# Kernel tuning notes

Measured on AMD Instinct MI355X. Metric: run time of the kernel, lower is better.

Reference implementation:

```python
import jax, jax.numpy as jnp
import numpy as np

B, T, C, H = 4096, 4, 1024, 8
DH = C // H
SCALE = DH ** -0.5
LN_EPS = 1e-5


def setup_inputs() -> dict:
    key = jax.random.key(0)
    k1, k2, k3 = jax.random.split(key, 3)
    feats = jax.random.normal(k1, (B, T, C), dtype=jnp.float32)
    Wqkv = jax.random.normal(k2, (T, C, 3 * C), dtype=jnp.float32) * 0.02
    bqkv = jnp.zeros((T, 3 * C), dtype=jnp.float32)
    Wproj = jax.random.normal(k3, (T, C, C), dtype=jnp.float32) * 0.02
    bproj = jnp.zeros((T, C), dtype=jnp.float32)
    gamma = jnp.ones((C,), dtype=jnp.float32)
    beta = jnp.zeros((C,), dtype=jnp.float32)
    return {"feats": feats, "Wqkv": Wqkv, "bqkv": bqkv,
            "Wproj": Wproj, "bproj": bproj, "gamma": gamma, "beta": beta}


def reference(feats, Wqkv, bqkv, Wproj, bproj, gamma, beta):
    # Grouped per-task QKV projection: [B,T,C] x [T,C,3C] -> [B,T,3C]
    qkv = jnp.einsum('btc,tcd->btd', feats, Wqkv) + bqkv
    q, k, v = jnp.split(qkv, 3, axis=-1)           # each [B,T,C]
    q = q.reshape(B, T, H, DH)
    k = k.reshape(B, T, H, DH)
    v = v.reshape(B, T, H, DH)
    # Cross-task attention: scores[b, query_task, key_task, head]
    scores = jnp.einsum('bqhd,bkhd->bqkh', q, k) * SCALE
    attn = jax.nn.softmax(scores, axis=2)          # softmax over key-task dim
    ctx = jnp.einsum('bqkh,bkhd->bqhd', attn, v)   # [B,T,H,DH]
    ctx = ctx.reshape(B, T, C)
    # Grouped per-task output projection (dropout is identity in eval)
    ctx = jnp.einsum('btc,tcd->btd', ctx, Wproj) + bproj
    # Residual + shared LayerNorm over channel dim
    x = ctx + feats
    mu = jnp.mean(x, axis=-1, keepdims=True)
    var = jnp.mean(jnp.square(x - mu), axis=-1, keepdims=True)
    return (x - mu) * jax.lax.rsqrt(var + LN_EPS) * gamma + beta
```

## Files before the change

### kernel.cpp

```cpp
#include <hip/hip_runtime.h>
#include <hip/hip_bf16.h>
#include <cstdint>
#include <cstddef>

#define B_SZ 4096
#define T_SZ 4
#define C_SZ 1024
#define H_SZ 8
#define DH_SZ 128
#define NQKV 3072
#define SCALE_F 0.08838834764831845f

typedef float f32x4 __attribute__((ext_vector_type(4)));
typedef short s16x8 __attribute__((ext_vector_type(8)));

static __device__ __forceinline__ float bf2f(unsigned short u) {
    union { unsigned int i; float f; } x; x.i = ((unsigned int)u) << 16; return x.f;
}
static __device__ __forceinline__ unsigned short f2bf(float f) {
    union { unsigned int i; float f; } x; x.f = f;
    unsigned int r = x.i + 0x7FFFu + ((x.i >> 16) & 1u);
    return (unsigned short)(r >> 16);
}

typedef const __attribute__((address_space(1))) void* gas_ptr;
typedef __attribute__((address_space(3))) void* las_ptr;
static __device__ __forceinline__ void async16(const void* g, void* l) {
    __builtin_amdgcn_global_load_lds((gas_ptr)g, (las_ptr)l, 16, 0, 0);
}

__global__ __launch_bounds__(256) void cvt_f32_bf16(const float* __restrict__ src,
                                                    unsigned short* __restrict__ dst, int n4) {
    int i = blockIdx.x * 256 + threadIdx.x;
    if (i >= n4) return;
    float4 v = reinterpret_cast<const float4*>(src)[i];
    ushort4 o;
    o.x = f2bf(v.x); o.y = f2bf(v.y); o.z = f2bf(v.z); o.w = f2bf(v.w);
    reinterpret_cast<ushort4*>(dst)[i] = o;
}

__global__ __launch_bounds__(256) void transpose_cvt(const float* __restrict__ src,
                                                     unsigned short* __restrict__ dst,
                                                     int K, int N) {
    __shared__ float tile[32][33];
    const float* s = src + (size_t)blockIdx.z * K * N;
    unsigned short* d = dst + (size_t)blockIdx.z * K * N;
    int n0 = blockIdx.x * 32, k0 = blockIdx.y * 32;
    int tx = threadIdx.x, ty = threadIdx.y;
#pragma unroll
    for (int i = 0; i < 4; i++) {
        int k = k0 + ty + i * 8;
        tile[ty + i * 8][tx] = s[(size_t)k * N + n0 + tx];
    }
    __syncthreads();
#pragma unroll
    for (int i = 0; i < 4; i++) {
        int n = n0 + ty + i * 8;
        d[(size_t)n * K + k0 + tx] = f2bf(tile[tx][ty + i * 8]);
    }
}

template<int NSIZE, int EPI>
__global__ __launch_bounds__(512, 1) void gemm256(
    const unsigned short* __restrict__ A,
    const unsigned short* __restrict__ Bt,
    const float* __restrict__ bias,
    const float* __restrict__ resid,
    unsigned short* __restrict__ out_bf,
    float* __restrict__ out_f)
{
    constexpr int BK  = 64;
    constexpr int NBX = NSIZE / 256;
    constexpr int NBY = B_SZ / 256;
    constexpr int NWG = NBX * NBY * T_SZ;

    __shared__ __align__(16) unsigned short lds[65536];

    const int bid = blockIdx.x;
    const int swz = (bid & 7) * (NWG >> 3) + (bid >> 3);
    const int by  = swz & (NBY - 1);
    const int tmp = swz >> 4;
    const int bx  = tmp % NBX;
    const int t   = tmp / NBX;
    const int m0  = by * 256;
    const int n0  = bx * 256;

    const int tid  = threadIdx.x;
    const int lane = tid & 63;
    const int w    = tid >> 6;
    const int wm   = w >> 2;
    const int wn   = w & 3;
    const int quad = lane >> 4;
    const int l16  = lane & 15;

    const int q0  = w * 128 + lane;
    const int q1  = q0 + 64;
    const int r0  = q0 >> 3, ch0 = (q0 & 7) ^ (r0 & 7);
    const int r1  = q1 >> 3, ch1 = (q1 & 7) ^ (r1 & 7);
    const unsigned short* Abase = A + (size_t)t * C_SZ;
    const unsigned short* Bbase = Bt + (size_t)t * NSIZE * C_SZ;
    const unsigned short* gA0 = Abase + (size_t)(m0 + r0) * (T_SZ * C_SZ) + ch0 * 8;
    const unsigned short* gA1 = Abase + (size_t)(m0 + r1) * (T_SZ * C_SZ) + ch1 * 8;
    const unsigned short* gB0 = Bbase + (size_t)(n0 + r0) * C_SZ + ch0 * 8;
    const unsigned short* gB1 = Bbase + (size_t)(n0 + r1) * C_SZ + ch1 * 8;
    unsigned short* dA0 = &lds[(w * 2 + 0) * 512];
    unsigned short* dA1 = &lds[(w * 2 + 1) * 512];
    unsigned short* dB0 = &lds[32768 + (w * 2 + 0) * 512];
    unsigned short* dB1 = &lds[32768 + (w * 2 + 1) * 512];

#define STG_A(buf, h, kt) do { \
    async16(gA0 + (size_t)(h) * 128 * (T_SZ * C_SZ) + (kt) * BK, dA0 + (buf) * 16384 + (h) * 8192); \
    async16(gA1 + (size_t)(h) * 128 * (T_SZ * C_SZ) + (kt) * BK, dA1 + (buf) * 16384 + (h) * 8192); \
} while (0)
#define STG_B(buf, h, kt) do { \
    async16(gB0 + (size_t)(h) * 128 * C_SZ + (kt) * BK, dB0 + (buf) * 16384 + (h) * 8192); \
    async16(gB1 + (size_t)(h) * 128 * C_SZ + (kt) * BK, dB1 + (buf) * 16384 + (h) * 8192); \
} while (0)

    const int s7   = l16 & 7;
    const int swk0 = ((0 * 4 + quad) ^ s7) * 8;
    const int swk1 = ((1 * 4 + quad) ^ s7) * 8;
    const unsigned short* aR = &lds[wm * 8192 + l16 * 64];
    const unsigned short* bR = &lds[32768 + (wn >> 1) * 8192 + ((wn & 1) * 64 + l16) * 64];

#define LD_A(buf, mh) do { \
    _Pragma("unroll") \
    for (int mi = 0; mi < 4; ++mi) { \
        af[mi][0] = *(const s16x8*)(aR + (buf) * 16384 + ((mh) * 4 + mi) * 1024 + swk0); \
        af[mi][1] = *(const s16x8*)(aR + (buf) * 16384 + ((mh) * 4 + mi) * 1024 + swk1); \
    } \
} while (0)
#define LD_B(buf, nh, dst) do { \
    _Pragma("unroll") \
    for (int ni = 0; ni < 2; ++ni) { \
        dst[ni][0] = *(const s16x8*)(bR + (buf) * 16384 + ((nh) * 2 + ni) * 1024 + swk0); \
        dst[ni][1] = *(const s16x8*)(bR + (buf) * 16384 + ((nh) * 2 + ni) * 1024 + swk1); \
    } \
} while (0)
#define MM(mh, nh, bsrc) do { \
    _Pragma("unroll") \
    for (int mi = 0; mi < 4; ++mi) \
    _Pragma("unroll") \
    for (int ni = 0; ni < 2; ++ni) { \
        acc[(mh) * 4 + mi][(nh) * 2 + ni] = __builtin_amdgcn_mfma_f32_16x16x32_bf16( \
            af[mi][0], bsrc[ni][0], acc[(mh) * 4 + mi][(nh) * 2 + ni], 0, 0, 0); \
        acc[(mh) * 4 + mi][(nh) * 2 + ni] = __builtin_amdgcn_mfma_f32_16x16x32_bf16( \
            af[mi][1], bsrc[ni][1], acc[(mh) * 4 + mi][(nh) * 2 + ni], 0, 0, 0); \
    } \
} while (0)
#define WALL() do { \
    __builtin_amdgcn_s_barrier(); \
    __builtin_amdgcn_sched_barrier(0); \
} while (0)
#define KTILE(buf, kt, SP0, SP23, VMC) do { \
     \
    asm volatile("s_waitcnt vmcnt(" #VMC ")"); \
    __builtin_amdgcn_sched_barrier(0); \
    WALL(); \
    LD_B(buf, 0, bq0); \
    LD_A(buf, 0); \
    LD_B(buf, 1, bq1); \
    if (SP0) STG_A((buf) ^ 1, 1, (kt) + 1); \
    __builtin_amdgcn_s_setprio(1); MM(0, 0, bq0); MM(0, 1, bq1); __builtin_amdgcn_s_setprio(0); \
     \
    WALL(); \
    LD_A(buf, 1); \
    if (SP23) { STG_B(buf, 0, (kt) + 2); STG_A(buf, 0, (kt) + 2); STG_B(buf, 1, (kt) + 2); } \
    __builtin_amdgcn_s_setprio(1); MM(1, 1, bq1); MM(1, 0, bq0); __builtin_amdgcn_s_setprio(0); \
} while (0)

    f32x4 acc[8][4] = {};
    s16x8 af[4][2], bq0[2][2], bq1[2][2];

    STG_A(0, 0, 0); STG_B(0, 0, 0); STG_B(0, 1, 0);
    STG_A(0, 1, 0);
    STG_B(1, 0, 1); STG_A(1, 0, 1); STG_B(1, 1, 1);

#pragma clang loop unroll(disable)
    for (int it = 0; it < 7; ++it) {
        int kt = it * 2;
        KTILE(0, kt,     1, 1, 6);
        KTILE(1, kt + 1, 1, 1, 6);
    }
    KTILE(0, 14, 1, 0, 6);
    KTILE(1, 15, 0, 0, 0);

#undef KTILE
#undef WALL
#undef MM
#undef LD_B
#undef LD_A
#undef STG_B
#undef STG_A

#pragma unroll
    for (int ni = 0; ni < 4; ++ni) {
        int gn = n0 + wn * 64 + ni * 16 + l16;
        float bi = bias[t * NSIZE + gn];
#pragma unroll
        for (int mi = 0; mi < 8; ++mi) {
#pragma unroll
            for (int r = 0; r < 4; ++r) {
                int gm = m0 + wm * 128 + mi * 16 + quad * 4 + r;
                size_t o = (size_t)(gm * T_SZ + t) * NSIZE + gn;
                float v = acc[mi][ni][r] + bi;
                if (EPI == 0) {
                    out_bf[o] = f2bf(v);
                } else {
                    out_f[o] = v + resid[o];
                }
            }
        }
    }
}

__global__ __launch_bounds__(256) void attn_kernel(const unsigned short* __restrict__ qkv,
                                                   unsigned short* __restrict__ ctx) {
    const int tid = threadIdx.x;
    const int li  = tid & 15;
    const int g   = blockIdx.x * 16 + (tid >> 4);
    const int b   = g >> 3, h = g & 7;
    const int d0  = li * 8;

    const unsigned short* base = qkv + (size_t)b * (T_SZ * NQKV) + h * DH_SZ + d0;
    float qf[4][8], kf[4][8], vf[4][8];
#pragma unroll
    for (int i = 0; i < 4; i++) {
        const unsigned short* p = base + (size_t)i * NQKV;
        s16x8 qv = *reinterpret_cast<const s16x8*>(p);
        s16x8 kv = *reinterpret_cast<const s16x8*>(p + C_SZ);
        s16x8 vv = *reinterpret_cast<const s16x8*>(p + 2 * C_SZ);
#pragma unroll
        for (int e = 0; e < 8; e++) {
            qf[i][e] = bf2f((unsigned short)qv[e]);
            kf[i][e] = bf2f((unsigned short)kv[e]);
            vf[i][e] = bf2f((unsigned short)vv[e]);
        }
    }
    float s[4][4];
#pragma unroll
    for (int i = 0; i < 4; i++)
#pragma unroll
        for (int j = 0; j < 4; j++) {
            float p = 0.0f;
#pragma unroll
            for (int e = 0; e < 8; e++) p += qf[i][e] * kf[j][e];
            p += __shfl_xor(p, 8);
            p += __shfl_xor(p, 4);
            p += __shfl_xor(p, 2);
            p += __shfl_xor(p, 1);
            s[i][j] = p * SCALE_F;
        }
#pragma unroll
    for (int i = 0; i < 4; i++) {
        float m = fmaxf(fmaxf(s[i][0], s[i][1]), fmaxf(s[i][2], s[i][3]));
        float e0 = __expf(s[i][0] - m), e1 = __expf(s[i][1] - m);
        float e2 = __expf(s[i][2] - m), e3 = __expf(s[i][3] - m);
        float inv = 1.0f / (e0 + e1 + e2 + e3);
        s[i][0] = e0 * inv; s[i][1] = e1 * inv; s[i][2] = e2 * inv; s[i][3] = e3 * inv;
    }
#pragma unroll
    for (int i = 0; i < 4; i++) {
        s16x8 ov;
#pragma unroll
        for (int e = 0; e < 8; e++) {
            float o = s[i][0] * vf[0][e] + s[i][1] * vf[1][e]
                    + s[i][2] * vf[2][e] + s[i][3] * vf[3][e];
            ov[e] = (short)f2bf(o);
        }
        *reinterpret_cast<s16x8*>(ctx + (size_t)(b * T_SZ + i) * C_SZ + h * DH_SZ + d0) = ov;
    }
}

__global__ __launch_bounds__(256) void ln_kernel(const float* __restrict__ y,
                                                 const float* __restrict__ gamma,
                                                 const float* __restrict__ beta,
                                                 float* __restrict__ out) {
    int row = blockIdx.x;
    int lane = threadIdx.x & 63, wave = threadIdx.x >> 6;
    float4 v = reinterpret_cast<const float4*>(y + (size_t)row * C_SZ)[threadIdx.x];
    float s  = v.x + v.y + v.z + v.w;
    float ss = v.x * v.x + v.y * v.y + v.z * v.z + v.w * v.w;
#pragma unroll
    for (int off = 32; off > 0; off >>= 1) { s += __shfl_xor(s, off); ss += __shfl_xor(ss, off); }
    __shared__ float red[8];
    if (lane == 0) { red[wave] = s; red[wave + 4] = ss; }
    __syncthreads();
    float S  = red[0] + red[1] + red[2] + red[3];
    float SS = red[4] + red[5] + red[6] + red[7];
    float mean = S * (1.0f / C_SZ);
    float var  = SS * (1.0f / C_SZ) - mean * mean;
    float inv  = rsqrtf(var + 1e-5f);
    float4 g  = reinterpret_cast<const float4*>(gamma)[threadIdx.x];
    float4 be = reinterpret_cast<const float4*>(beta)[threadIdx.x];
    float4 o;
    o.x = (v.x - mean) * inv * g.x + be.x;
    o.y = (v.y - mean) * inv * g.y + be.y;
    o.z = (v.z - mean) * inv * g.z + be.z;
    o.w = (v.w - mean) * inv * g.w + be.w;
    reinterpret_cast<float4*>(out + (size_t)row * C_SZ)[threadIdx.x] = o;
}

extern "C" void kernel_launch(void* const* d_in, const int* in_sizes, int n_in,
                              void* d_out, int out_size, void* d_ws, size_t ws_size,
                              hipStream_t stream) {
    const float* feats = (const float*)d_in[0];
    const float* Wqkv  = (const float*)d_in[1];
    const float* bqkv  = (const float*)d_in[2];
    const float* Wproj = (const float*)d_in[3];
    const float* bproj = (const float*)d_in[4];
    const float* gamma = (const float*)d_in[5];
    const float* beta  = (const float*)d_in[6];
    float* out = (float*)d_out;

    char* ws = (char*)d_ws;
    unsigned short* feats_bf = (unsigned short*)(ws);
    unsigned short* wqkv_t   = (unsigned short*)(ws + 33554432);
    unsigned short* wproj_t  = (unsigned short*)(ws + 58720256);
    unsigned short* qkv      = (unsigned short*)(ws + 67108864);
    unsigned short* ctx      = (unsigned short*)(ws + 167772160);
    float* ybuf              = (float*)(ws + 67108864);

    cvt_f32_bf16<<<16384, 256, 0, stream>>>(feats, feats_bf, (B_SZ * T_SZ * C_SZ) / 4);
    transpose_cvt<<<dim3(96, 32, 4), dim3(32, 8), 0, stream>>>(Wqkv, wqkv_t, C_SZ, NQKV);
    transpose_cvt<<<dim3(32, 32, 4), dim3(32, 8), 0, stream>>>(Wproj, wproj_t, C_SZ, C_SZ);

    gemm256<NQKV, 0><<<dim3(768), 512, 0, stream>>>(
        feats_bf, wqkv_t, bqkv, nullptr, qkv, nullptr);

    attn_kernel<<<(B_SZ * H_SZ) / 16, 256, 0, stream>>>(qkv, ctx);

    gemm256<C_SZ, 1><<<dim3(256), 512, 0, stream>>>(
        ctx, wproj_t, bproj, feats, nullptr, ybuf);

    ln_kernel<<<B_SZ * T_SZ, 256, 0, stream>>>(ybuf, gamma, beta, out);
}
```

Before: 405.4 us.

## Emit bf16 from output projection and fuse residual into wave-per-row LayerNorm

The output-projection GEMM now writes bf16 instead of fp32 with a residual read, and the residual add moves into a new LayerNorm kernel that handles one row per wave with no shared-memory reduction. The weight transpose processes 64-row tiles and writes packed ushort2 pairs, and the feature conversion uses a grid-stride loop with fewer blocks. These changes cut GEMM epilogue traffic and launch and synchronisation overhead. Rounding the pre-LayerNorm projection output to bf16 adds some precision loss.

```diff
diff --git a/kernel.cpp b/kernel.cpp
--- a/kernel.cpp
+++ b/kernel.cpp
@@ -31,24 +31,25 @@
 
 __global__ __launch_bounds__(256) void cvt_f32_bf16(const float* __restrict__ src,
                                                     unsigned short* __restrict__ dst, int n4) {
-    int i = blockIdx.x * 256 + threadIdx.x;
-    if (i >= n4) return;
-    float4 v = reinterpret_cast<const float4*>(src)[i];
-    ushort4 o;
-    o.x = f2bf(v.x); o.y = f2bf(v.y); o.z = f2bf(v.z); o.w = f2bf(v.w);
-    reinterpret_cast<ushort4*>(dst)[i] = o;
+    int stride = gridDim.x * 256;
+    for (int i = blockIdx.x * 256 + threadIdx.x; i < n4; i += stride) {
+        float4 v = reinterpret_cast<const float4*>(src)[i];
+        ushort4 o;
+        o.x = f2bf(v.x); o.y = f2bf(v.y); o.z = f2bf(v.z); o.w = f2bf(v.w);
+        reinterpret_cast<ushort4*>(dst)[i] = o;
+    }
 }
 
 __global__ __launch_bounds__(256) void transpose_cvt(const float* __restrict__ src,
                                                      unsigned short* __restrict__ dst,
                                                      int K, int N) {
-    __shared__ float tile[32][33];
+    __shared__ float tile[64][33];
     const float* s = src + (size_t)blockIdx.z * K * N;
     unsigned short* d = dst + (size_t)blockIdx.z * K * N;
-    int n0 = blockIdx.x * 32, k0 = blockIdx.y * 32;
+    int n0 = blockIdx.x * 32, k0 = blockIdx.y * 64;
     int tx = threadIdx.x, ty = threadIdx.y;
 #pragma unroll
-    for (int i = 0; i < 4; i++) {
+    for (int i = 0; i < 8; i++) {
         int k = k0 + ty + i * 8;
         tile[ty + i * 8][tx] = s[(size_t)k * N + n0 + tx];
     }
@@ -56,18 +57,19 @@
 #pragma unroll
     for (int i = 0; i < 4; i++) {
         int n = n0 + ty + i * 8;
-        d[(size_t)n * K + k0 + tx] = f2bf(tile[tx][ty + i * 8]);
-    }
-}
-
-template<int NSIZE, int EPI>
+        ushort2 o;
+        o.x = f2bf(tile[2 * tx][ty + i * 8]);
+        o.y = f2bf(tile[2 * tx + 1][ty + i * 8]);
+        *reinterpret_cast<ushort2*>(&d[(size_t)n * K + k0 + 2 * tx]) = o;
+    }
+}
+
+template<int NSIZE>
 __global__ __launch_bounds__(512, 1) void gemm256(
     const unsigned short* __restrict__ A,
     const unsigned short* __restrict__ Bt,
     const float* __restrict__ bias,
-    const float* __restrict__ resid,
-    unsigned short* __restrict__ out_bf,
-    float* __restrict__ out_f)
+    unsigned short* __restrict__ out_bf)
 {
     constexpr int BK  = 64;
     constexpr int NBX = NSIZE / 256;
@@ -203,12 +205,7 @@
             for (int r = 0; r < 4; ++r) {
                 int gm = m0 + wm * 128 + mi * 16 + quad * 4 + r;
                 size_t o = (size_t)(gm * T_SZ + t) * NSIZE + gn;
-                float v = acc[mi][ni][r] + bi;
-                if (EPI == 0) {
-                    out_bf[o] = f2bf(v);
-                } else {
-                    out_f[o] = v + resid[o];
-                }
+                out_bf[o] = f2bf(acc[mi][ni][r] + bi);
             }
         }
     }
@@ -272,33 +269,47 @@
     }
 }
 
-__global__ __launch_bounds__(256) void ln_kernel(const float* __restrict__ y,
-                                                 const float* __restrict__ gamma,
-                                                 const float* __restrict__ beta,
-                                                 float* __restrict__ out) {
-    int row = blockIdx.x;
-    int lane = threadIdx.x & 63, wave = threadIdx.x >> 6;
-    float4 v = reinterpret_cast<const float4*>(y + (size_t)row * C_SZ)[threadIdx.x];
-    float s  = v.x + v.y + v.z + v.w;
-    float ss = v.x * v.x + v.y * v.y + v.z * v.z + v.w * v.w;
+__global__ __launch_bounds__(256) void ln_fused(const unsigned short* __restrict__ yb,
+                                                const float* __restrict__ feats,
+                                                const float* __restrict__ gamma,
+                                                const float* __restrict__ beta,
+                                                float* __restrict__ out) {
+    const int wave = threadIdx.x >> 6, lane = threadIdx.x & 63;
+    const int row = blockIdx.x * 4 + wave;
+    const unsigned short* yp = yb + (size_t)row * C_SZ;
+    const float* fp = feats + (size_t)row * C_SZ;
+
+    float x[4][4];
+    float s = 0.0f, ss = 0.0f;
+#pragma unroll
+    for (int c = 0; c < 4; c++) {
+        int col = c * 256 + lane * 4;
+        ushort4 u = *reinterpret_cast<const ushort4*>(yp + col);
+        float4 f = *reinterpret_cast<const float4*>(fp + col);
+        x[c][0] = bf2f(u.x) + f.x;
+        x[c][1] = bf2f(u.y) + f.y;
+        x[c][2] = bf2f(u.z) + f.z;
+        x[c][3] = bf2f(u.w) + f.w;
+#pragma unroll
+        for (int j = 0; j < 4; j++) { s += x[c][j]; ss += x[c][j] * x[c][j]; }
+    }
 #pragma unroll
     for (int off = 32; off > 0; off >>= 1) { s += __shfl_xor(s, off); ss += __shfl_xor(ss, off); }
-    __shared__ float red[8];
-    if (lane == 0) { red[wave] = s; red[wave + 4] = ss; }
-    __syncthreads();
-    float S  = red[0] + red[1] + red[2] + red[3];
-    float SS = red[4] + red[5] + red[6] + red[7];
-    float mean = S * (1.0f / C_SZ);
-    float var  = SS * (1.0f / C_SZ) - mean * mean;
+    float mean = s * (1.0f / C_SZ);
+    float var  = ss * (1.0f / C_SZ) - mean * mean;
     float inv  = rsqrtf(var + 1e-5f);
-    float4 g  = reinterpret_cast<const float4*>(gamma)[threadIdx.x];
-    float4 be = reinterpret_cast<const float4*>(beta)[threadIdx.x];
-    float4 o;
-    o.x = (v.x - mean) * inv * g.x + be.x;
-    o.y = (v.y - mean) * inv * g.y + be.y;
-    o.z = (v.z - mean) * inv * g.z + be.z;
-    o.w = (v.w - mean) * inv * g.w + be.w;
-    reinterpret_cast<float4*>(out + (size_t)row * C_SZ)[threadIdx.x] = o;
+#pragma unroll
+    for (int c = 0; c < 4; c++) {
+        int col = c * 256 + lane * 4;
+        float4 g  = *reinterpret_cast<const float4*>(gamma + col);
+        float4 be = *reinterpret_cast<const float4*>(beta + col);
+        float4 o;
+        o.x = (x[c][0] - mean) * inv * g.x + be.x;
+        o.y = (x[c][1] - mean) * inv * g.y + be.y;
+        o.z = (x[c][2] - mean) * inv * g.z + be.z;
+        o.w = (x[c][3] - mean) * inv * g.w + be.w;
+        *reinterpret_cast<float4*>(out + (size_t)row * C_SZ + col) = o;
+    }
 }
 
 extern "C" void kernel_launch(void* const* d_in, const int* in_sizes, int n_in,
@@ -319,19 +330,17 @@
     unsigned short* wproj_t  = (unsigned short*)(ws + 58720256);
     unsigned short* qkv      = (unsigned short*)(ws + 67108864);
     unsigned short* ctx      = (unsigned short*)(ws + 167772160);
-    float* ybuf              = (float*)(ws + 67108864);
-
-    cvt_f32_bf16<<<16384, 256, 0, stream>>>(feats, feats_bf, (B_SZ * T_SZ * C_SZ) / 4);
-    transpose_cvt<<<dim3(96, 32, 4), dim3(32, 8), 0, stream>>>(Wqkv, wqkv_t, C_SZ, NQKV);
-    transpose_cvt<<<dim3(32, 32, 4), dim3(32, 8), 0, stream>>>(Wproj, wproj_t, C_SZ, C_SZ);
-
-    gemm256<NQKV, 0><<<dim3(768), 512, 0, stream>>>(
-        feats_bf, wqkv_t, bqkv, nullptr, qkv, nullptr);
+    unsigned short* ybuf_bf  = (unsigned short*)(ws + 67108864);
+
+    cvt_f32_bf16<<<2048, 256, 0, stream>>>(feats, feats_bf, (B_SZ * T_SZ * C_SZ) / 4);
+    transpose_cvt<<<dim3(96, 16, 4), dim3(32, 8), 0, stream>>>(Wqkv, wqkv_t, C_SZ, NQKV);
+    transpose_cvt<<<dim3(32, 16, 4), dim3(32, 8), 0, stream>>>(Wproj, wproj_t, C_SZ, C_SZ);
+
+    gemm256<NQKV><<<dim3(768), 512, 0, stream>>>(feats_bf, wqkv_t, bqkv, qkv);
 
     attn_kernel<<<(B_SZ * H_SZ) / 16, 256, 0, stream>>>(qkv, ctx);
 
-    gemm256<C_SZ, 1><<<dim3(256), 512, 0, stream>>>(
-        ctx, wproj_t, bproj, feats, nullptr, ybuf);
-
-    ln_kernel<<<B_SZ * T_SZ, 256, 0, stream>>>(ybuf, gamma, beta, out);
-}
+    gemm256<C_SZ><<<dim3(256), 512, 0, stream>>>(ctx, wproj_t, bproj, ybuf_bf);
+
+    ln_fused<<<(B_SZ * T_SZ) / 4, 256, 0, stream>>>(ybuf_bf, feats, gamma, beta, out);
+}
```

Result: faster. 387.0 us (-4.5%).
